# Optimization experiments

Measured on AMD Instinct MI355X. Metric: run time of the kernel, lower is better.

Reference implementation:

```python
import jax, jax.numpy as jnp
import numpy as np

# db4 decomposition filters (as in get_wavelet_filters('db4'))
_H0 = jnp.array([0.0322231, -0.01260397, -0.09921954, 0.2978578,
                 0.80373875, 0.49761867, -0.02963553, -0.07576571], dtype=jnp.float32)
_H1 = jnp.array([0.07576571, -0.02963553, -0.49761867, 0.80373875,
                 -0.2978578, -0.09921954, 0.01260397, 0.0322231], dtype=jnp.float32)
LEVEL = 2
IN_CH, OUT_CH, MODES = 64, 64, 32


def subband_conv2d(x, k2d, stride):
    # depthwise (grouped) conv: same 2D filter applied per channel, NHWC
    C = x.shape[-1]
    k = jnp.tile(k2d[:, :, None, None], (1, 1, 1, C)).astype(x.dtype)  # HWIO, I=1
    return jax.lax.conv_general_dilated(
        x, k, (stride, stride), 'SAME',
        dimension_numbers=('NHWC', 'HWIO', 'NHWC'), feature_group_count=C)


def upsample2d(t):
    B, H, W, C = t.shape
    return jnp.zeros((B, 2 * H, 2 * W, C), t.dtype).at[:, ::2, ::2, :].set(t)


def setup_inputs() -> dict:
    key = jax.random.key(0)
    kx, k1, k2, k3, k4 = jax.random.split(key, 5)
    scale = 1.0 / (IN_CH * OUT_CH)
    wshape = (IN_CH, OUT_CH, MODES, MODES)
    return {
        'x': jax.random.normal(kx, (32, 128, 128, IN_CH), dtype=jnp.float32),
        'weights1': scale * jax.random.uniform(k1, wshape, dtype=jnp.float32),
        'weights2': scale * jax.random.uniform(k2, wshape, dtype=jnp.float32),
        'weights3': scale * jax.random.uniform(k3, wshape, dtype=jnp.float32),
        'weights4': scale * jax.random.uniform(k4, wshape, dtype=jnp.float32),
    }


def reference(x, weights1, weights2, weights3, weights4):
    # H=W=128 == size and divisible by 2**LEVEL: pad branch and effective_level
    # adjustment in the original are no-ops.
    h0, h1 = _H0, _H1
    g0, g1 = h0[::-1], h1[::-1]  # reconstruction filters

    # ---- multi-level 2D DWT (depthwise strided convs per subband) ----
    approx = x
    details = []
    for _ in range(LEVEL):
        lh = subband_conv2d(approx, jnp.outer(h0, h1), 2)
        hl = subband_conv2d(approx, jnp.outer(h1, h0), 2)
        hh = subband_conv2d(approx, jnp.outer(h1, h1), 2)
        approx = subband_conv2d(approx, jnp.outer(h0, h0), 2)
        details.append((lh, hl, hh))

    # ---- per-pixel channel mixing on final LL and last-level details ----
    ah, aw = approx.shape[1], approx.shape[2]
    out_ft = jnp.einsum('bhwi,iohw->bhwo', approx, weights1[:, :, :ah, :aw])
    last_lh, last_hl, last_hh = details[-1]
    dh, dw = last_lh.shape[1], last_lh.shape[2]
    out_lh = jnp.einsum('bhwi,iohw->bhwo', last_lh, weights2[:, :, :dh, :dw])
    out_hl = jnp.einsum('bhwi,iohw->bhwo', last_hl, weights3[:, :, :dh, :dw])
    out_hh = jnp.einsum('bhwi,iohw->bhwo', last_hh, weights4[:, :, :dh, :dw])

    # ---- IDWT reconstruction ----
    # Deepest level: all four subbands contribute. Earlier levels: details are
    # zeroed in the original, and conv(zeros)=0, so only the LL path remains.
    res = (subband_conv2d(upsample2d(out_ft), jnp.outer(g0, g0), 1)
           + subband_conv2d(upsample2d(out_lh), jnp.outer(g0, g1), 1)
           + subband_conv2d(upsample2d(out_hl), jnp.outer(g1, g0), 1)
           + subband_conv2d(upsample2d(out_hh), jnp.outer(g1, g1), 1))
    for _ in range(LEVEL - 1):
        res = subband_conv2d(upsample2d(res), jnp.outer(g0, g0), 1)
    return res
```

## Files before the change

### kernel.cpp

```cpp
#include <hip/hip_runtime.h>


__constant__ float c_h0[8] = {0.0322231f, -0.01260397f, -0.09921954f, 0.2978578f,
                              0.80373875f, 0.49761867f, -0.02963553f, -0.07576571f};
__constant__ float c_h1[8] = {0.07576571f, -0.02963553f, -0.49761867f, 0.80373875f,
                              -0.2978578f, -0.09921954f, 0.01260397f, 0.0322231f};
__constant__ float c_g0[8] = {-0.07576571f, -0.02963553f, 0.49761867f, 0.80373875f,
                              0.2978578f, -0.09921954f, -0.01260397f, 0.0322231f};
__constant__ float c_g1[8] = {0.0322231f, 0.01260397f, -0.09921954f, -0.2978578f,
                              0.80373875f, -0.49761867f, -0.02963553f, 0.07576571f};

__device__ __forceinline__ float4 f4z() { return make_float4(0.f, 0.f, 0.f, 0.f); }
__device__ __forceinline__ float4 f4fma(float4 a, float w, float4 v) {
  a.x = fmaf(w, v.x, a.x); a.y = fmaf(w, v.y, a.y);
  a.z = fmaf(w, v.z, a.z); a.w = fmaf(w, v.w, a.w);
  return a;
}

__global__ __launch_bounds__(256) void k_dwt1t(const float* __restrict__ x,
                                               float* __restrict__ ll1,
                                               const float* __restrict__ w1,
                                               const float* __restrict__ w2,
                                               const float* __restrict__ w3,
                                               const float* __restrict__ w4,
                                               float* __restrict__ wt) {
  __shared__ float4 sRow[4][40 * 17];
  int t = threadIdx.x;
  int bid = blockIdx.x;

  if (bid >= 512) {
    int bid2 = bid - 512;
    int s   = bid2 >> 10;
    int rem = bid2 & 1023;
    int hw0 = (rem & 15) << 6;
    int io0 = (rem >> 4) << 6;
    const float* w = (s == 0) ? w1 : (s == 1) ? w2 : (s == 2) ? w3 : w4;
    float* tile = (float*)sRow;
    int c = t & 15;
    int r = t >> 4;
#pragma unroll
    for (int k = 0; k < 4; ++k) {
      int io = r + 16 * k;
      float4 v = *(const float4*)(w + (size_t)(io0 + io) * 1024 + hw0 + c * 4);
      tile[io * 65 + c * 4 + 0] = v.x;
      tile[io * 65 + c * 4 + 1] = v.y;
      tile[io * 65 + c * 4 + 2] = v.z;
      tile[io * 65 + c * 4 + 3] = v.w;
    }
    __syncthreads();
    float* o = wt + (size_t)s * 4194304;
#pragma unroll
    for (int k = 0; k < 4; ++k) {
      int hr = r + 16 * k;
      float4 v;
      v.x = tile[(c * 4 + 0) * 65 + hr];
      v.y = tile[(c * 4 + 1) * 65 + hr];
      v.z = tile[(c * 4 + 2) * 65 + hr];
      v.w = tile[(c * 4 + 3) * 65 + hr];
      *(float4*)(o + (size_t)(hw0 + hr) * 4096 + io0 + c * 4) = v;
    }
    return;
  }

  int c4 = t & 15;
  int owl = t >> 4;
  int owb = bid & 3;
  int ohc = (bid >> 2) & 3;
  int b   = bid >> 4;
  int ow0 = owb * 16;
  int ow  = ow0 + owl;
  int oh0 = ohc * 16;
  int iw_start = 2 * ow0 - 3;
  const float* xb = x + ((size_t)b << 20);

  auto stageN = [&](int ih0, int nrows) {
    int items = nrows * 40;
    for (int base = 0; base < items; base += 16) {
      int item = base + owl;
      int rw   = item / 40;
      int iw_s = item - rw * 40;
      int ihc  = min(max(ih0 + rw, 0), 127);
      int iwc  = min(max(iw_start + iw_s, 0), 127);
      sRow[rw][iw_s * 17 + c4] =
          *(const float4*)(xb + (size_t)ihc * 8192 + (iwc << 6) + (c4 << 2));
    }
  };

  auto hrowL = [&](int rw, int ih) -> float4 {
    float4 r = f4z();
    if ((unsigned)ih >= 128u) return r;
#pragma unroll
    for (int j = 0; j < 8; ++j) {
      int iw  = 2 * ow - 3 + j;
      int iwc = min(max(iw, 0), 127);
      int iw_s = iwc - iw_start;
      float w = ((unsigned)iw < 128u) ? c_h0[j] : 0.f;
      r = f4fma(r, w, sRow[rw][iw_s * 17 + c4]);
    }
    return r;
  };

  float4 ring[10];
  int ihb = 2 * oh0 - 3;
  stageN(ihb, 4);
  __syncthreads();
#pragma unroll
  for (int k = 0; k < 4; ++k) ring[k] = hrowL(k, ihb + k);
  __syncthreads();
  stageN(ihb + 4, 4);
  __syncthreads();
#pragma unroll
  for (int k = 0; k < 4; ++k) ring[4 + k] = hrowL(k, ihb + 4 + k);
  __syncthreads();

  float* outp = ll1 + ((((size_t)b * 64 + oh0) * 64 + ow) << 6) + (c4 << 2);
#pragma unroll
  for (int p = 0; p < 8; ++p) {
    int nfill = (p == 0) ? 2 : 4;
    int fill0 = 10 - nfill;
    stageN(ihb + 4 * p + fill0, nfill);
    __syncthreads();
#pragma unroll
    for (int k = 0; k < 4; ++k) {
      if (k < nfill) ring[fill0 + k] = hrowL(k, ihb + 4 * p + fill0 + k);
    }
    float4 a0 = f4z(), a1 = f4z();
#pragma unroll
    for (int i = 0; i < 8; ++i) {
      a0 = f4fma(a0, c_h0[i], ring[i]);
      a1 = f4fma(a1, c_h0[i], ring[i + 2]);
    }
    *(float4*)(outp + (2 * p) * 4096)     = a0;
    *(float4*)(outp + (2 * p + 1) * 4096) = a1;
    __syncthreads();
#pragma unroll
    for (int k = 0; k < 6; ++k) ring[k] = ring[k + 4];
  }
}

__global__ __launch_bounds__(256) void k_dwt2(const float* __restrict__ ll1,
                                              float* __restrict__ subs) {
  __shared__ float4 sRow[2][40 * 17];
  int t = threadIdx.x;
  int c4 = t & 15;
  int owl = t >> 4;
  int bid = blockIdx.x;
  int owb = bid & 1;
  int ohc = (bid >> 1) & 7;
  int b   = bid >> 4;
  int ow0 = owb * 16;
  int ow  = ow0 + owl;
  int oh0 = ohc * 4;
  int iw_start = 2 * ow0 - 3;
  const float* lb = ll1 + ((size_t)b << 18);

  auto stage2 = [&](int ih0) {
#pragma unroll
    for (int base = 0; base < 80; base += 16) {
      int item = base + owl;
      int rw   = item >= 40 ? 1 : 0;
      int iw_s = item - rw * 40;
      int ihc  = min(max(ih0 + rw, 0), 63);
      int iwc  = min(max(iw_start + iw_s, 0), 63);
      sRow[rw][iw_s * 17 + c4] =
          *(const float4*)(lb + (size_t)ihc * 4096 + (iwc << 6) + (c4 << 2));
    }
  };

  auto hrow2L = [&](int rw, int ih, float4& rl, float4& rh) {
    rl = f4z(); rh = f4z();
    if ((unsigned)ih >= 64u) return;
#pragma unroll
    for (int j = 0; j < 8; ++j) {
      int iw  = 2 * ow - 3 + j;
      int iwc = min(max(iw, 0), 63);
      int iw_s = iwc - iw_start;
      bool ok = (unsigned)iw < 64u;
      float wl = ok ? c_h0[j] : 0.f;
      float wh = ok ? c_h1[j] : 0.f;
      float4 v = sRow[rw][iw_s * 17 + c4];
      rl = f4fma(rl, wl, v);
      rh = f4fma(rh, wh, v);
    }
  };

  float4 Rl[8], Rh[8];
  int ihb = 2 * oh0 - 3;
#pragma unroll
  for (int pk = 0; pk < 3; ++pk) {
    stage2(ihb + 2 * pk);
    __syncthreads();
    hrow2L(0, ihb + 2 * pk,     Rl[2 * pk],     Rh[2 * pk]);
    hrow2L(1, ihb + 2 * pk + 1, Rl[2 * pk + 1], Rh[2 * pk + 1]);
    __syncthreads();
  }
  float* outp = subs + ((((size_t)b * 32 + oh0) * 32 + ow) << 6) + (c4 << 2);
#pragma unroll
  for (int oo = 0; oo < 4; ++oo) {
    stage2(ihb + 6);
    __syncthreads();
    hrow2L(0, ihb + 6, Rl[6], Rh[6]);
    hrow2L(1, ihb + 7, Rl[7], Rh[7]);
    float4 a_ll = f4z(), a_lh = f4z(), a_hl = f4z(), a_hh = f4z();
#pragma unroll
    for (int i = 0; i < 8; ++i) {
      a_ll = f4fma(a_ll, c_h0[i], Rl[i]);
      a_lh = f4fma(a_lh, c_h0[i], Rh[i]);
      a_hl = f4fma(a_hl, c_h1[i], Rl[i]);
      a_hh = f4fma(a_hh, c_h1[i], Rh[i]);
    }
    float* o = outp + oo * 2048;
    *(float4*)(o)           = a_ll;
    *(float4*)(o + 2097152) = a_lh;
    *(float4*)(o + 4194304) = a_hl;
    *(float4*)(o + 6291456) = a_hh;
    __syncthreads();
#pragma unroll
    for (int k = 0; k < 6; ++k) { Rl[k] = Rl[k + 2]; Rh[k] = Rh[k + 2]; }
    ihb += 2;
  }
}

__global__ __launch_bounds__(256) void k_einsum(const float* __restrict__ subs,
                                               const float* __restrict__ w1,
                                               const float* __restrict__ w2,
                                               const float* __restrict__ w3,
                                               const float* __restrict__ w4,
                                               const float* __restrict__ wt,
                                               float* __restrict__ eout,
                                               int use_wt) {
  __shared__ float sW[4096];
  __shared__ float sA[2048];
  int p = blockIdx.x;
  int s = blockIdx.y;
  int t = threadIdx.x;
  const float* A = subs + (size_t)s * 2097152;
  if (use_wt) {
    const float* Wp = wt + (size_t)s * 4194304 + (size_t)p * 4096;
#pragma unroll
    for (int k = 0; k < 16; ++k) sW[t + 256 * k] = Wp[t + 256 * k];
  } else {
    const float* Ws = (s == 0) ? w1 : (s == 1) ? w2 : (s == 2) ? w3 : w4;
#pragma unroll
    for (int k = 0; k < 16; ++k) {
      int e = t + 256 * k;
      sW[e] = Ws[e * 1024 + p];
    }
  }
#pragma unroll
  for (int k = 0; k < 8; ++k) {
    int e = t + 256 * k;
    sA[e] = A[(e >> 6) * 65536 + (p << 6) + (e & 63)];
  }
  __syncthreads();
  int o  = t & 63;
  int bg = t >> 6;
  float acc[8] = {0.f, 0.f, 0.f, 0.f, 0.f, 0.f, 0.f, 0.f};
  for (int i = 0; i < 64; ++i) {
    float wv = sW[(i << 6) + o];
#pragma unroll
    for (int k = 0; k < 8; ++k) acc[k] += sA[((bg * 8 + k) << 6) + i] * wv;
  }
  float* Oo = eout + (size_t)s * 2097152 + (p << 6) + o;
#pragma unroll
  for (int k = 0; k < 8; ++k) Oo[(bg * 8 + k) * 65536] = acc[k];
}

__global__ __launch_bounds__(256) void k_invfinal(const float* __restrict__ eout,
                                                  float* __restrict__ out) {
  __shared__ float4 sRes[3][2][20][16];
  int t = threadIdx.x;
  int c4 = t & 15;
  int ql = t >> 4;
  int bid = blockIdx.x;
  int xt = bid & 3;
  int yt = (bid >> 2) & 3;
  int b  = bid >> 4;
  int q0 = xt * 16;
  int qi0 = (q0 >> 1) - 1;
  int qi = qi0 + ql;
  int r0p = yt * 8;

  auto loadrowI = [&](int m, float4& ae, float4& ao, float4& be, float4& bo) {
    ae = f4z(); ao = f4z(); be = f4z(); bo = f4z();
    if ((unsigned)m >= 32u) return;
    const float* base = eout + ((((size_t)b * 32 + m) * 32) << 6) + (c4 << 2);
    float4 vf[4], vl[4], vh[4], vv[4];
#pragma unroll
    for (int dn = -1; dn <= 2; ++dn) {
      int n = qi + dn;
      int nc = min(max(n, 0), 31);
      const float* p = base + (nc << 6);
      vf[dn + 1] = *(const float4*)(p);
      vl[dn + 1] = *(const float4*)(p + 2097152);
      vh[dn + 1] = *(const float4*)(p + 4194304);
      vv[dn + 1] = *(const float4*)(p + 6291456);
    }
#pragma unroll
    for (int dn = -1; dn <= 2; ++dn) {
      int n = qi + dn;
      bool ok = (unsigned)n < 32u;
      float g0e = ok ? c_g0[2 * dn + 3] : 0.f, g1e = ok ? c_g1[2 * dn + 3] : 0.f;
      float g0o = ok ? c_g0[2 * dn + 2] : 0.f, g1o = ok ? c_g1[2 * dn + 2] : 0.f;
      ae = f4fma(ae, g0e, vf[dn + 1]); ae = f4fma(ae, g1e, vl[dn + 1]);
      ao = f4fma(ao, g0o, vf[dn + 1]); ao = f4fma(ao, g1o, vl[dn + 1]);
      be = f4fma(be, g0e, vh[dn + 1]); be = f4fma(be, g1e, vv[dn + 1]);
      bo = f4fma(bo, g0o, vh[dn + 1]); bo = f4fma(bo, g1o, vv[dn + 1]);
    }
  };

  float4 Ae[4], Ao[4], Be[4], Bo[4];
  int prs = r0p - 1;

  auto steppair = [&]() {
    loadrowI(prs + 2, Ae[3], Ao[3], Be[3], Bo[3]);
    float4 ee = f4z(), eo = f4z(), oe = f4z(), oo = f4z();
    if ((unsigned)prs < 32u) {
#pragma unroll
      for (int dm = 0; dm < 4; ++dm) {
        float gye = c_g0[2 * dm + 1], hye = c_g1[2 * dm + 1];
        float gyo = c_g0[2 * dm],     hyo = c_g1[2 * dm];
        ee = f4fma(ee, gye, Ae[dm]); ee = f4fma(ee, hye, Be[dm]);
        eo = f4fma(eo, gye, Ao[dm]); eo = f4fma(eo, hye, Bo[dm]);
        oe = f4fma(oe, gyo, Ae[dm]); oe = f4fma(oe, hyo, Be[dm]);
        oo = f4fma(oo, gyo, Ao[dm]); oo = f4fma(oo, hyo, Bo[dm]);
      }
    }
    int slot = ((prs % 3) + 3) % 3;
    sRes[slot][0][2 * ql][c4]     = ee;
    sRes[slot][0][2 * ql + 1][c4] = eo;
    sRes[slot][1][2 * ql][c4]     = oe;
    sRes[slot][1][2 * ql + 1][c4] = oo;
#pragma unroll
    for (int k = 0; k < 3; ++k) {
      Ae[k] = Ae[k + 1]; Ao[k] = Ao[k + 1]; Be[k] = Be[k + 1]; Bo[k] = Bo[k + 1];
    }
  };

  if (ql < 10) {
    loadrowI(prs - 1, Ae[0], Ao[0], Be[0], Bo[0]);
    loadrowI(prs,     Ae[1], Ao[1], Be[1], Bo[1]);
    loadrowI(prs + 1, Ae[2], Ao[2], Be[2], Bo[2]);
  }
#pragma unroll
  for (int pk = 0; pk < 2; ++pk) {
    if (ql < 10) steppair();
    ++prs;
  }
  int q = q0 + ql;
#pragma unroll
  for (int it = 0; it < 8; ++it) {
    if (ql < 10) steppair();
    __syncthreads();
    float4 H0[5], H1[5];
#pragma unroll
    for (int mi = 0; mi < 5; ++mi) {
      int m = 2 * (prs - 1) - 1 + mi;
      int pm = m >> 1;
      int ey = m & 1;
      int slot = ((pm % 3) + 3) % 3;
      float4 h0v = f4z(), h1v = f4z();
#pragma unroll
      for (int dn = -1; dn <= 2; ++dn) {
        int n = q + dn;
        bool ok = (unsigned)n < 64u;
        float we = ok ? c_g0[2 * dn + 3] : 0.f;
        float wo = ok ? c_g0[2 * dn + 2] : 0.f;
        float4 v = sRes[slot][ey][ql + 2 + dn][c4];
        h0v = f4fma(h0v, we, v);
        h1v = f4fma(h1v, wo, v);
      }
      H0[mi] = h0v; H1[mi] = h1v;
    }
#pragma unroll
    for (int rr2 = 0; rr2 < 2; ++rr2) {
      int r = 2 * (prs - 1) + rr2;
      float4 aee = f4z(), aeo = f4z(), aoe = f4z(), aoo = f4z();
#pragma unroll
      for (int dm = 0; dm < 4; ++dm) {
        float gye = c_g0[2 * dm + 1];
        float gyo = c_g0[2 * dm];
        aee = f4fma(aee, gye, H0[rr2 + dm]);
        aeo = f4fma(aeo, gye, H1[rr2 + dm]);
        aoe = f4fma(aoe, gyo, H0[rr2 + dm]);
        aoo = f4fma(aoo, gyo, H1[rr2 + dm]);
      }
      int y = 2 * r, xx = 2 * q;
      float* ob = out + (((size_t)(b * 128 + y)) * 128 + xx) * 64 + (c4 << 2);
      *(float4*)(ob)              = aee;
      *(float4*)(ob + 64)         = aeo;
      *(float4*)(ob + 8192)       = aoe;
      *(float4*)(ob + 8192 + 64)  = aoo;
    }
    __syncthreads();
    ++prs;
  }
}

extern "C" void kernel_launch(void* const* d_in, const int* in_sizes, int n_in,
                              void* d_out, int out_size, void* d_ws, size_t ws_size,
                              hipStream_t stream) {
  (void)in_sizes; (void)n_in; (void)out_size;
  const float* x  = (const float*)d_in[0];
  const float* w1 = (const float*)d_in[1];
  const float* w2 = (const float*)d_in[2];
  const float* w3 = (const float*)d_in[3];
  const float* w4 = (const float*)d_in[4];
  float* out = (float*)d_out;
  float* ws  = (float*)d_ws;

  float* ll1  = ws;
  float* subs = ws + 8388608;
  float* eout = ws + 16777216;
  float* wt   = ws + 25165824;
  int use_wt = (ws_size >= (size_t)41943040 * 4) ? 1 : 0;

  int g1 = use_wt ? (512 + 4096) : 512;
  k_dwt1t<<<g1, 256, 0, stream>>>(x, ll1, w1, w2, w3, w4, wt);
  k_dwt2<<<512, 256, 0, stream>>>(ll1, subs);
  k_einsum<<<dim3(1024, 4), 256, 0, stream>>>(subs, w1, w2, w3, w4, wt, eout, use_wt);
  k_invfinal<<<512, 256, 0, stream>>>(eout, out);
}
```

Before: 364.9 us.

## Split level-1 DWT into separate horizontal and vertical pass kernels

Replaces the fused level-1 LL kernel, which used an LDS-staged ring buffer, with two simple separable kernels. A horizontal pass writes a 32x128x64x64 intermediate to workspace, and a vertical pass reads it back to produce ll1. The weight transpose moves into its own kernel. The aim is more parallelism and less LDS staging and sync overhead, at the cost of an extra full-size intermediate written to and read from global memory (about 64MB of traffic).

```diff
diff --git a/kernel.cpp b/kernel.cpp
--- a/kernel.cpp
+++ b/kernel.cpp
@@ -17,124 +17,98 @@
   return a;
 }
 
-__global__ __launch_bounds__(256) void k_dwt1t(const float* __restrict__ x,
-                                               float* __restrict__ ll1,
-                                               const float* __restrict__ w1,
-                                               const float* __restrict__ w2,
-                                               const float* __restrict__ w3,
-                                               const float* __restrict__ w4,
-                                               float* __restrict__ wt) {
-  __shared__ float4 sRow[4][40 * 17];
-  int t = threadIdx.x;
-  int bid = blockIdx.x;
-
-  if (bid >= 512) {
-    int bid2 = bid - 512;
-    int s   = bid2 >> 10;
-    int rem = bid2 & 1023;
-    int hw0 = (rem & 15) << 6;
-    int io0 = (rem >> 4) << 6;
-    const float* w = (s == 0) ? w1 : (s == 1) ? w2 : (s == 2) ? w3 : w4;
-    float* tile = (float*)sRow;
-    int c = t & 15;
-    int r = t >> 4;
-#pragma unroll
-    for (int k = 0; k < 4; ++k) {
-      int io = r + 16 * k;
-      float4 v = *(const float4*)(w + (size_t)(io0 + io) * 1024 + hw0 + c * 4);
-      tile[io * 65 + c * 4 + 0] = v.x;
-      tile[io * 65 + c * 4 + 1] = v.y;
-      tile[io * 65 + c * 4 + 2] = v.z;
-      tile[io * 65 + c * 4 + 3] = v.w;
-    }
-    __syncthreads();
-    float* o = wt + (size_t)s * 4194304;
-#pragma unroll
-    for (int k = 0; k < 4; ++k) {
-      int hr = r + 16 * k;
-      float4 v;
-      v.x = tile[(c * 4 + 0) * 65 + hr];
-      v.y = tile[(c * 4 + 1) * 65 + hr];
-      v.z = tile[(c * 4 + 2) * 65 + hr];
-      v.w = tile[(c * 4 + 3) * 65 + hr];
-      *(float4*)(o + (size_t)(hw0 + hr) * 4096 + io0 + c * 4) = v;
-    }
-    return;
-  }
-
+__global__ __launch_bounds__(256) void k_dwt1h(const float* __restrict__ x,
+                                               float* __restrict__ t1) {
+  int t = threadIdx.x;
   int c4 = t & 15;
   int owl = t >> 4;
+  int bid = blockIdx.x;
   int owb = bid & 3;
-  int ohc = (bid >> 2) & 3;
-  int b   = bid >> 4;
-  int ow0 = owb * 16;
-  int ow  = ow0 + owl;
-  int oh0 = ohc * 16;
-  int iw_start = 2 * ow0 - 3;
-  const float* xb = x + ((size_t)b << 20);
-
-  auto stageN = [&](int ih0, int nrows) {
-    int items = nrows * 40;
-    for (int base = 0; base < items; base += 16) {
-      int item = base + owl;
-      int rw   = item / 40;
-      int iw_s = item - rw * 40;
-      int ihc  = min(max(ih0 + rw, 0), 127);
-      int iwc  = min(max(iw_start + iw_s, 0), 127);
-      sRow[rw][iw_s * 17 + c4] =
-          *(const float4*)(xb + (size_t)ihc * 8192 + (iwc << 6) + (c4 << 2));
-    }
-  };
-
-  auto hrowL = [&](int rw, int ih) -> float4 {
-    float4 r = f4z();
-    if ((unsigned)ih >= 128u) return r;
-#pragma unroll
-    for (int j = 0; j < 8; ++j) {
-      int iw  = 2 * ow - 3 + j;
-      int iwc = min(max(iw, 0), 127);
-      int iw_s = iwc - iw_start;
-      float w = ((unsigned)iw < 128u) ? c_h0[j] : 0.f;
-      r = f4fma(r, w, sRow[rw][iw_s * 17 + c4]);
-    }
-    return r;
-  };
-
-  float4 ring[10];
-  int ihb = 2 * oh0 - 3;
-  stageN(ihb, 4);
+  int ih  = (bid >> 2) & 127;
+  int b   = bid >> 9;
+  int ow  = owb * 16 + owl;
+  const float* row = x + ((size_t)b << 20) + (size_t)ih * 8192 + (c4 << 2);
+  int iwbase = 2 * ow - 3;
+  float4 v[8];
+#pragma unroll
+  for (int j = 0; j < 8; ++j) {
+    int iw = iwbase + j;
+    int iwc = min(max(iw, 0), 127);
+    v[j] = *(const float4*)(row + (iwc << 6));
+  }
+  float4 r = f4z();
+#pragma unroll
+  for (int j = 0; j < 8; ++j) {
+    int iw = iwbase + j;
+    float w = ((unsigned)iw < 128u) ? c_h0[j] : 0.f;
+    r = f4fma(r, w, v[j]);
+  }
+  *(float4*)(t1 + ((((size_t)b * 128 + ih) * 64 + ow) << 6) + (c4 << 2)) = r;
+}
+
+__global__ __launch_bounds__(256) void k_dwt1v(const float* __restrict__ t1,
+                                               float* __restrict__ ll1) {
+  int t = threadIdx.x;
+  int c4 = t & 15;
+  int owl = t >> 4;
+  int bid = blockIdx.x;
+  int owb = bid & 3;
+  int oh  = (bid >> 2) & 63;
+  int b   = bid >> 8;
+  int ow  = owb * 16 + owl;
+  const float* col = t1 + ((size_t)b << 19) + ((size_t)ow << 6) + (c4 << 2);
+  int ihbase = 2 * oh - 3;
+  float4 v[8];
+#pragma unroll
+  for (int i = 0; i < 8; ++i) {
+    int ihc = min(max(ihbase + i, 0), 127);
+    v[i] = *(const float4*)(col + ((size_t)ihc << 12));
+  }
+  float4 r = f4z();
+#pragma unroll
+  for (int i = 0; i < 8; ++i) {
+    int ihh = ihbase + i;
+    float w = ((unsigned)ihh < 128u) ? c_h0[i] : 0.f;
+    r = f4fma(r, w, v[i]);
+  }
+  *(float4*)(ll1 + ((((size_t)b * 64 + oh) * 64 + ow) << 6) + (c4 << 2)) = r;
+}
+
+__global__ __launch_bounds__(256) void k_transpose(const float* __restrict__ w1,
+                                                   const float* __restrict__ w2,
+                                                   const float* __restrict__ w3,
+                                                   const float* __restrict__ w4,
+                                                   float* __restrict__ wt) {
+  __shared__ float tile[64 * 65];
+  int t = threadIdx.x;
+  int bid = blockIdx.x;
+  int s   = bid >> 10;
+  int rem = bid & 1023;
+  int hw0 = (rem & 15) << 6;
+  int io0 = (rem >> 4) << 6;
+  const float* w = (s == 0) ? w1 : (s == 1) ? w2 : (s == 2) ? w3 : w4;
+  int c = t & 15;
+  int r = t >> 4;
+#pragma unroll
+  for (int k = 0; k < 4; ++k) {
+    int io = r + 16 * k;
+    float4 v = *(const float4*)(w + (size_t)(io0 + io) * 1024 + hw0 + c * 4);
+    tile[io * 65 + c * 4 + 0] = v.x;
+    tile[io * 65 + c * 4 + 1] = v.y;
+    tile[io * 65 + c * 4 + 2] = v.z;
+    tile[io * 65 + c * 4 + 3] = v.w;
+  }
   __syncthreads();
-#pragma unroll
-  for (int k = 0; k < 4; ++k) ring[k] = hrowL(k, ihb + k);
-  __syncthreads();
-  stageN(ihb + 4, 4);
-  __syncthreads();
-#pragma unroll
-  for (int k = 0; k < 4; ++k) ring[4 + k] = hrowL(k, ihb + 4 + k);
-  __syncthreads();
-
-  float* outp = ll1 + ((((size_t)b * 64 + oh0) * 64 + ow) << 6) + (c4 << 2);
-#pragma unroll
-  for (int p = 0; p < 8; ++p) {
-    int nfill = (p == 0) ? 2 : 4;
-    int fill0 = 10 - nfill;
-    stageN(ihb + 4 * p + fill0, nfill);
-    __syncthreads();
-#pragma unroll
-    for (int k = 0; k < 4; ++k) {
-      if (k < nfill) ring[fill0 + k] = hrowL(k, ihb + 4 * p + fill0 + k);
-    }
-    float4 a0 = f4z(), a1 = f4z();
-#pragma unroll
-    for (int i = 0; i < 8; ++i) {
-      a0 = f4fma(a0, c_h0[i], ring[i]);
-      a1 = f4fma(a1, c_h0[i], ring[i + 2]);
-    }
-    *(float4*)(outp + (2 * p) * 4096)     = a0;
-    *(float4*)(outp + (2 * p + 1) * 4096) = a1;
-    __syncthreads();
-#pragma unroll
-    for (int k = 0; k < 6; ++k) ring[k] = ring[k + 4];
+  float* o = wt + (size_t)s * 4194304;
+#pragma unroll
+  for (int k = 0; k < 4; ++k) {
+    int hr = r + 16 * k;
+    float4 v;
+    v.x = tile[(c * 4 + 0) * 65 + hr];
+    v.y = tile[(c * 4 + 1) * 65 + hr];
+    v.z = tile[(c * 4 + 2) * 65 + hr];
+    v.w = tile[(c * 4 + 3) * 65 + hr];
+    *(float4*)(o + (size_t)(hw0 + hr) * 4096 + io0 + c * 4) = v;
   }
 }
 
@@ -410,13 +384,15 @@
   float* ws  = (float*)d_ws;
 
   float* ll1  = ws;
+  float* t1   = ws + 8388608;
   float* subs = ws + 8388608;
   float* eout = ws + 16777216;
   float* wt   = ws + 25165824;
   int use_wt = (ws_size >= (size_t)41943040 * 4) ? 1 : 0;
 
-  int g1 = use_wt ? (512 + 4096) : 512;
-  k_dwt1t<<<g1, 256, 0, stream>>>(x, ll1, w1, w2, w3, w4, wt);
+  k_dwt1h<<<16384, 256, 0, stream>>>(x, t1);
+  if (use_wt) k_transpose<<<4096, 256, 0, stream>>>(w1, w2, w3, w4, wt);
+  k_dwt1v<<<8192, 256, 0, stream>>>(t1, ll1);
   k_dwt2<<<512, 256, 0, stream>>>(ll1, subs);
   k_einsum<<<dim3(1024, 4), 256, 0, stream>>>(subs, w1, w2, w3, w4, wt, eout, use_wt);
   k_invfinal<<<512, 256, 0, stream>>>(eout, out);
```

Result: slower. 388.1 us (+6.3%).
